# Optimization experiments

Measured on AMD Instinct MI355X. Metric: run time of the kernel, lower is better.

The kernel has to match this reference:

```python
import jax, jax.numpy as jnp
import numpy as np

SEQ, IN, H = 8192, 1024, 2048

def setup_inputs() -> dict:
    key = jax.random.key(0)
    ks = jax.random.split(key, 7)
    s = 0.02
    return {
        "input_seq": jax.random.normal(ks[0], (SEQ, IN), jnp.float32),
        "W_ih": jax.random.normal(ks[1], (4 * H, IN), jnp.float32) * s,
        "W_hh": jax.random.normal(ks[2], (4 * H, H), jnp.float32) * s,
        "b_ih": jax.random.normal(ks[3], (4 * H,), jnp.float32) * s,
        "b_hh": jax.random.normal(ks[4], (4 * H,), jnpp if False else jnp.float32) * s if False else jax.random.normal(ks[4], (4 * H,), jnp.float32) * s,
        "W_lin": jax.random.normal(ks[5], (1, H), jnp.float32) * s,
        "b_lin": jax.random.normal(ks[6], (1,), jnp.float32) * s,
    }

def _lstm(input_seq, W_ih, W_hh, b, H):
    # Precompute input projections for all timesteps: [S, 4H]
    x_proj = input_seq @ W_ih.T + b

    def step(carry, xp):
        h, c = carry
        gates = xp + h @ W_hh.T  # [4H], PyTorch order: i, f, g, o
        i = jax.nn.sigmoid(gates[0:H])
        f = jax.nn.sigmoid(gates[H:2 * H])
        g = jnp.tanh(gates[2 * H:3 * H])
        o = jax.nn.sigmoid(gates[3 * H:4 * H])
        c = f * c + i * g
        h = o * jnp.tanh(c)
        return (h, c), h

    h0 = jnp.zeros((H,), input_seq.dtype)
    c0 = jnp.zeros((H,), input_seq.dtype)
    _, hs = jax.lax.scan(step, (h0, c0), x_proj)
    return hs  # [S, H]

def reference(input_seq, W_ih, W_hh, b_ih, b_hh, W_lin, b_lin):
    H_ = W_hh.shape[1]
    hs = _lstm(input_seq, W_ih, W_hh, b_ih + b_hh, H_)
    # dropout is identity in eval mode; then linear + sigmoid + flatten
    out = jax.nn.sigmoid(hs @ W_lin.T + b_lin)  # [S, 1]
    return out.reshape(-1)
```

## Files before the change

### kernel.cpp

```cpp
#include <hip/hip_runtime.h>
#include <hip/hip_bf16.h>
#include <stdint.h>

constexpr int kSEQ = 8192;
constexpr int kIN  = 1024;
constexpr int kH   = 2048;
constexpr int kG4  = 4 * kH;
constexpr int kNB  = 256;
constexpr int kHB  = kH / kNB;
constexpr int kWP  = kH + 16;

constexpr size_t OFF_HBUF  = 0;
constexpr size_t OFF_ABORT = 32768;
constexpr size_t OFF_HS    = 65536;
constexpr size_t OFF_XP    = OFF_HS + (size_t)kSEQ * kH * 2;

__device__ __forceinline__ float bflo(uint32_t v) { return __uint_as_float(v << 16); }
__device__ __forceinline__ float bfhi(uint32_t v) { return __uint_as_float(v & 0xffff0000u); }

__global__ __launch_bounds__(256) void k_xproj(const float* __restrict__ A,
                                               const float* __restrict__ B,
                                               const float* __restrict__ bih,
                                               const float* __restrict__ bhh,
                                               __hip_bfloat16* __restrict__ C)
{
    __shared__ float As[16][65];
    __shared__ float Bs[16][65];

    const int bx = blockIdx.x & 127;
    const int by = blockIdx.x >> 7;
    const int tid = threadIdx.x;
    const int r  = tid >> 2;
    const int kq = (tid & 3) << 2;
    const int tx = tid & 15;
    const int ty = tid >> 4;
    const int m0 = by * 64, n0 = bx * 64;

    float acc[4][4] = {};

    for (int k0 = 0; k0 < kIN; k0 += 16) {
        float4 av = *(const float4*)&A[(size_t)(m0 + r) * kIN + k0 + kq];
        float4 bv = *(const float4*)&B[(size_t)(n0 + r) * kIN + k0 + kq];
        __syncthreads();
        As[kq + 0][r] = av.x; As[kq + 1][r] = av.y; As[kq + 2][r] = av.z; As[kq + 3][r] = av.w;
        Bs[kq + 0][r] = bv.x; Bs[kq + 1][r] = bv.y; Bs[kq + 2][r] = bv.z; Bs[kq + 3][r] = bv.w;
        __syncthreads();
        #pragma unroll
        for (int k = 0; k < 16; ++k) {
            float a0 = As[k][ty * 4 + 0], a1 = As[k][ty * 4 + 1];
            float a2 = As[k][ty * 4 + 2], a3 = As[k][ty * 4 + 3];
            float b0 = Bs[k][tx * 4 + 0], b1 = Bs[k][tx * 4 + 1];
            float b2 = Bs[k][tx * 4 + 2], b3 = Bs[k][tx * 4 + 3];
            acc[0][0] += a0 * b0; acc[0][1] += a0 * b1; acc[0][2] += a0 * b2; acc[0][3] += a0 * b3;
            acc[1][0] += a1 * b0; acc[1][1] += a1 * b1; acc[1][2] += a1 * b2; acc[1][3] += a1 * b3;
            acc[2][0] += a2 * b0; acc[2][1] += a2 * b1; acc[2][2] += a2 * b2; acc[2][3] += a2 * b3;
            acc[3][0] += a3 * b0; acc[3][1] += a3 * b1; acc[3][2] += a3 * b2; acc[3][3] += a3 * b3;
        }
    }

    #pragma unroll
    for (int i = 0; i < 4; ++i) {
        const int m = m0 + ty * 4 + i;
        #pragma unroll
        for (int j = 0; j < 4; ++j) {
            const int n = n0 + tx * 4 + j;
            C[(size_t)m * kG4 + n] = __float2bfloat16(acc[i][j] + bih[n] + bhh[n]);
        }
    }
}

__global__ __launch_bounds__(256, 1) void k_lstm(const float* __restrict__ Whh,
                                                 const __hip_bfloat16* __restrict__ xp,
                                                 unsigned long long* __restrict__ hbuf,
                                                 uint32_t* __restrict__ abortf,
                                                 __hip_bfloat16* __restrict__ hs)
{
    extern __shared__ char smem[];
    __hip_bfloat16* Wl  = (__hip_bfloat16*)smem;
    float*          hl2 = (float*)(smem + 32 * kWP * 2);

    const int wg  = blockIdx.x;
    const int tid = threadIdx.x;
    const int w   = tid >> 6;
    const int l   = tid & 63;
    const int hb  = wg * kHB;

    {
        const int lr = tid >> 3;
        const int g  = lr & 3;
        const int jl = 2 * (lr >> 3) + ((lr >> 2) & 1);
        const int cb = (tid & 7) * 256;
        const float* src = Whh + (size_t)(g * kH + hb + jl) * kH + cb;
        __hip_bfloat16* dst = Wl + (size_t)lr * kWP + cb;
        for (int c = 0; c < 256; c += 4) {
            float4 v = *(const float4*)(src + c);
            dst[c + 0] = __float2bfloat16(v.x);
            dst[c + 1] = __float2bfloat16(v.y);
            dst[c + 2] = __float2bfloat16(v.z);
            dst[c + 3] = __float2bfloat16(v.w);
        }
    }
    __syncthreads();

    const __hip_bfloat16* wrow = Wl + (size_t)(w * 8 + (l >> 3)) * kWP;
    const int kbase = (l & 7) * 8;
    const int jg = hb + 2 * w + (l >> 5);
    float c_state = 0.0f;
    uint32_t budget = 0;

    for (int t = 0; t < kSEQ; ++t) {
        const __hip_bfloat16* xr = xp + (size_t)t * kG4 + jg;
        const float xi = __bfloat162float(xr[0]);
        const float xf = __bfloat162float(xr[kH]);
        const float xg = __bfloat162float(xr[2 * kH]);
        const float xo = __bfloat162float(xr[3 * kH]);

        float* hw = hl2 + (size_t)(t & 1) * kH + tid * 8;
        int dead = 0;
        if (t == 0) {
            #pragma unroll
            for (int j = 0; j < 8; ++j) hw[j] = 0.f;
        } else {
            const unsigned long long* src = hbuf + (size_t)((t - 1) & 1) * kH + tid * 8;
            const uint32_t tag = (uint32_t)t;
            unsigned long long v[8];
            for (;;) {
                #pragma unroll
                for (int j = 0; j < 8; ++j)
                    v[j] = __hip_atomic_load(src + j, __ATOMIC_RELAXED, __HIP_MEMORY_SCOPE_AGENT);
                bool ok = true;
                #pragma unroll
                for (int j = 0; j < 8; ++j) ok &= ((uint32_t)v[j] == tag);
                if (ok) break;
                if ((++budget & 15) == 0) {
                    if (__hip_atomic_load(abortf, __ATOMIC_RELAXED,
                                          __HIP_MEMORY_SCOPE_AGENT) != 0u) { dead = 1; break; }
                    if (budget > (1u << 21)) {
                        __hip_atomic_store(abortf, 1u, __ATOMIC_RELAXED,
                                           __HIP_MEMORY_SCOPE_AGENT);
                        dead = 1; break;
                    }
                }
            }
            #pragma unroll
            for (int j = 0; j < 8; ++j) hw[j] = __uint_as_float((uint32_t)(v[j] >> 32));
        }
        if (__syncthreads_or(dead)) return;

        const float* hv = hl2 + (size_t)(t & 1) * kH;
        float acc = 0.f;
        #pragma unroll 8
        for (int it = 0; it < 32; ++it) {
            const int k = it * 64 + kbase;
            uint4 wv = *(const uint4*)(wrow + k);
            float4 h0 = *(const float4*)(hv + k);
            float4 h1 = *(const float4*)(hv + k + 4);
            acc += bflo(wv.x) * h0.x + bfhi(wv.x) * h0.y
                 + bflo(wv.y) * h0.z + bfhi(wv.y) * h0.w
                 + bflo(wv.z) * h1.x + bfhi(wv.z) * h1.y
                 + bflo(wv.w) * h1.z + bfhi(wv.w) * h1.w;
        }
        acc += __shfl_xor(acc, 1);
        acc += __shfl_xor(acc, 2);
        acc += __shfl_xor(acc, 4);

        const int base = l & 32;
        const float gi = __shfl(acc, base + 0)  + xi;
        const float gf = __shfl(acc, base + 8)  + xf;
        const float gg = __shfl(acc, base + 16) + xg;
        const float go = __shfl(acc, base + 24) + xo;
        const float si = 1.f / (1.f + expf(-gi));
        const float sf = 1.f / (1.f + expf(-gf));
        const float tg = tanhf(gg);
        const float so = 1.f / (1.f + expf(-go));
        c_state = sf * c_state + si * tg;
        const float hvv = so * tanhf(c_state);
        if ((l & 31) == 0) {
            hs[(size_t)t * kH + jg] = __float2bfloat16(hvv);
            const unsigned long long pv =
                ((unsigned long long)__float_as_uint(hvv) << 32) | (uint32_t)(t + 1);
            __hip_atomic_store(hbuf + (size_t)(t & 1) * kH + jg, pv,
                               __ATOMIC_RELAXED, __HIP_MEMORY_SCOPE_AGENT);
        }
    }
}

__global__ __launch_bounds__(256) void k_out(const __hip_bfloat16* __restrict__ hs,
                                             const float* __restrict__ wlin,
                                             const float* __restrict__ blin,
                                             float* __restrict__ out)
{
    const int w = threadIdx.x >> 6, l = threadIdx.x & 63;
    const int t = blockIdx.x * 4 + w;
    const __hip_bfloat16* row = hs + (size_t)t * kH;
    float acc = 0.f;
    #pragma unroll
    for (int i = 0; i < 4; ++i) {
        const int k = i * 512 + l * 8;
        uint4 hv = *(const uint4*)(row + k);
        float4 w0 = *(const float4*)(wlin + k);
        float4 w1 = *(const float4*)(wlin + k + 4);
        acc += bflo(hv.x) * w0.x + bfhi(hv.x) * w0.y
             + bflo(hv.y) * w0.z + bfhi(hv.y) * w0.w
             + bflo(hv.z) * w1.x + bfhi(hv.z) * w1.y
             + bflo(hv.w) * w1.z + bfhi(hv.w) * w1.w;
    }
    #pragma unroll
    for (int s = 32; s >= 1; s >>= 1) acc += __shfl_xor(acc, s);
    if (l == 0) out[t] = 1.f / (1.f + expf(-(acc + blin[0])));
}

extern "C" void kernel_launch(void* const* d_in, const int* in_sizes, int n_in,
                              void* d_out, int out_size, void* d_ws, size_t ws_size,
                              hipStream_t stream)
{
    const float* input_seq = (const float*)d_in[0];
    const float* W_ih      = (const float*)d_in[1];
    const float* W_hh      = (const float*)d_in[2];
    const float* b_ih      = (const float*)d_in[3];
    const float* b_hh      = (const float*)d_in[4];
    const float* W_lin     = (const float*)d_in[5];
    const float* b_lin     = (const float*)d_in[6];
    float* out = (float*)d_out;
    char*  ws  = (char*)d_ws;

    unsigned long long* hbuf = (unsigned long long*)(ws + OFF_HBUF);
    uint32_t*           abf  = (uint32_t*)(ws + OFF_ABORT);
    __hip_bfloat16*     hs   = (__hip_bfloat16*)(ws + OFF_HS);
    __hip_bfloat16*     xpb  = (__hip_bfloat16*)(ws + OFF_XP);

    hipMemsetAsync(ws, 0, 65536, stream);

    k_xproj<<<dim3(128 * 128), dim3(256), 0, stream>>>(input_seq, W_ih, b_ih, b_hh, xpb);

    constexpr int kLds = 32 * kWP * 2 + 2 * kH * 4;
    hipFuncSetAttribute((const void*)k_lstm, hipFuncAttributeMaxDynamicSharedMemorySize, kLds);

    {
        const float* a0 = W_hh; const __hip_bfloat16* a1 = xpb;
        unsigned long long* a2 = hbuf; uint32_t* a3 = abf; __hip_bfloat16* a4 = hs;
        void* args[5] = { &a0, &a1, &a2, &a3, &a4 };
        hipError_t ce = hipLaunchCooperativeKernel((const void*)k_lstm, dim3(kNB), dim3(256),
                                                   args, (unsigned)kLds, stream);
        if (ce != hipSuccess) {
            k_lstm<<<dim3(kNB), dim3(256), kLds, stream>>>(W_hh, xpb, hbuf, abf, hs);
        }
    }

    k_out<<<dim3(kSEQ / 4), dim3(256), 0, stream>>>(hs, W_lin, b_lin, out);
}
```

Before: 60.05 ms.

## Gate LSTM step on a global arrival counter before reading tagged h values

Adds a global atomic counter that every workgroup increments after publishing its h slice for a step. A single thread per workgroup polls that counter with s_sleep until all 256 groups have arrived, then all threads read the tagged hbuf once, with a per-element fallback spin. This replaces having every thread spin on 8 atomic loads, which is meant to cut polling traffic on the shared cache. It adds an extra __syncthreads and a contended atomic add per step, plus sleep latency on the critical path of a latency-bound recurrence.

```diff
diff --git a/kernel.cpp b/kernel.cpp
--- a/kernel.cpp
+++ b/kernel.cpp
@@ -12,6 +12,7 @@
 
 constexpr size_t OFF_HBUF  = 0;
 constexpr size_t OFF_ABORT = 32768;
+constexpr size_t OFF_CNT   = 33024;
 constexpr size_t OFF_HS    = 65536;
 constexpr size_t OFF_XP    = OFF_HS + (size_t)kSEQ * kH * 2;
 
@@ -73,6 +74,7 @@
                                                  const __hip_bfloat16* __restrict__ xp,
                                                  unsigned long long* __restrict__ hbuf,
                                                  uint32_t* __restrict__ abortf,
+                                                 uint32_t* __restrict__ cnt,
                                                  __hip_bfloat16* __restrict__ hs)
 {
     extern __shared__ char smem[];
@@ -120,32 +122,59 @@
         if (t == 0) {
             #pragma unroll
             for (int j = 0; j < 8; ++j) hw[j] = 0.f;
+            __syncthreads();
         } else {
+            if (tid == 0) {
+                const uint32_t want = (uint32_t)t * 256u;
+                for (;;) {
+                    uint32_t c = __hip_atomic_load(cnt, __ATOMIC_RELAXED,
+                                                   __HIP_MEMORY_SCOPE_AGENT);
+                    if (c >= want) break;
+                    __builtin_amdgcn_s_sleep(2);
+                    if ((++budget & 15) == 0) {
+                        if (__hip_atomic_load(abortf, __ATOMIC_RELAXED,
+                                              __HIP_MEMORY_SCOPE_AGENT) != 0u) { dead = 1; break; }
+                        if (budget > (1u << 20)) {
+                            __hip_atomic_store(abortf, 1u, __ATOMIC_RELAXED,
+                                               __HIP_MEMORY_SCOPE_AGENT);
+                            dead = 1; break;
+                        }
+                    }
+                }
+            }
+            if (__syncthreads_or(dead)) return;
+
             const unsigned long long* src = hbuf + (size_t)((t - 1) & 1) * kH + tid * 8;
             const uint32_t tag = (uint32_t)t;
             unsigned long long v[8];
-            for (;;) {
-                #pragma unroll
-                for (int j = 0; j < 8; ++j)
-                    v[j] = __hip_atomic_load(src + j, __ATOMIC_RELAXED, __HIP_MEMORY_SCOPE_AGENT);
-                bool ok = true;
-                #pragma unroll
-                for (int j = 0; j < 8; ++j) ok &= ((uint32_t)v[j] == tag);
-                if (ok) break;
-                if ((++budget & 15) == 0) {
-                    if (__hip_atomic_load(abortf, __ATOMIC_RELAXED,
-                                          __HIP_MEMORY_SCOPE_AGENT) != 0u) { dead = 1; break; }
-                    if (budget > (1u << 21)) {
-                        __hip_atomic_store(abortf, 1u, __ATOMIC_RELAXED,
-                                           __HIP_MEMORY_SCOPE_AGENT);
-                        dead = 1; break;
+            #pragma unroll
+            for (int j = 0; j < 8; ++j)
+                v[j] = __hip_atomic_load(src + j, __ATOMIC_RELAXED, __HIP_MEMORY_SCOPE_AGENT);
+            bool ok = true;
+            #pragma unroll
+            for (int j = 0; j < 8; ++j) ok &= ((uint32_t)v[j] == tag);
+            if (!ok) {
+                #pragma unroll 1
+                for (int j = 0; j < 8 && !dead; ++j) {
+                    while ((uint32_t)v[j] != tag) {
+                        v[j] = __hip_atomic_load(src + j, __ATOMIC_RELAXED,
+                                                 __HIP_MEMORY_SCOPE_AGENT);
+                        if ((++budget & 255) == 0) {
+                            if (__hip_atomic_load(abortf, __ATOMIC_RELAXED,
+                                                  __HIP_MEMORY_SCOPE_AGENT) != 0u ||
+                                budget > (1u << 20)) {
+                                __hip_atomic_store(abortf, 1u, __ATOMIC_RELAXED,
+                                                   __HIP_MEMORY_SCOPE_AGENT);
+                                dead = 1; break;
+                            }
+                        }
                     }
                 }
             }
             #pragma unroll
             for (int j = 0; j < 8; ++j) hw[j] = __uint_as_float((uint32_t)(v[j] >> 32));
-        }
-        if (__syncthreads_or(dead)) return;
+            if (__syncthreads_or(dead)) return;
+        }
 
         const float* hv = hl2 + (size_t)(t & 1) * kH;
         float acc = 0.f;
@@ -182,6 +211,9 @@
             __hip_atomic_store(hbuf + (size_t)(t & 1) * kH + jg, pv,
                                __ATOMIC_RELAXED, __HIP_MEMORY_SCOPE_AGENT);
         }
+        __syncthreads();
+        if (tid == 0)
+            __hip_atomic_fetch_add(cnt, 1u, __ATOMIC_RELAXED, __HIP_MEMORY_SCOPE_AGENT);
     }
 }
 
@@ -226,6 +258,7 @@
 
     unsigned long long* hbuf = (unsigned long long*)(ws + OFF_HBUF);
     uint32_t*           abf  = (uint32_t*)(ws + OFF_ABORT);
+    uint32_t*           cnt  = (uint32_t*)(ws + OFF_CNT);
     __hip_bfloat16*     hs   = (__hip_bfloat16*)(ws + OFF_HS);
     __hip_bfloat16*     xpb  = (__hip_bfloat16*)(ws + OFF_XP);
 
@@ -238,12 +271,13 @@
 
     {
         const float* a0 = W_hh; const __hip_bfloat16* a1 = xpb;
-        unsigned long long* a2 = hbuf; uint32_t* a3 = abf; __hip_bfloat16* a4 = hs;
-        void* args[5] = { &a0, &a1, &a2, &a3, &a4 };
+        unsigned long long* a2 = hbuf; uint32_t* a3 = abf; uint32_t* a4 = cnt;
+        __hip_bfloat16* a5 = hs;
+        void* args[6] = { &a0, &a1, &a2, &a3, &a4, &a5 };
         hipError_t ce = hipLaunchCooperativeKernel((const void*)k_lstm, dim3(kNB), dim3(256),
                                                    args, (unsigned)kLds, stream);
         if (ce != hipSuccess) {
-            k_lstm<<<dim3(kNB), dim3(256), kLds, stream>>>(W_hh, xpb, hbuf, abf, hs);
+            k_lstm<<<dim3(kNB), dim3(256), kLds, stream>>>(W_hh, xpb, hbuf, abf, cnt, hs);
         }
     }
 
```

After: 75.27 ms. 1.25x slower.

## Replace per-step block barrier with per-chunk LDS counters for streaming h consumption

Applied to the files above, without the earlier changes.

Removes the __syncthreads_or barrier after each wave loads its slice of the previous hidden state. In its place, every 8-thread group bumps a per-chunk LDS counter (double-buffered by step parity), and the dot-product loop spin-waits on each chunk's counter before reading it. The goal is to let waves start the matvec as soon as the chunks they need have arrived, so the global-poll latency overlaps with compute instead of serialising at a block barrier. The cost is extra LDS atomics and acquire loads inside the inner loop, a smaller unroll, and more complex abort handling.

```diff
diff --git a/kernel.cpp b/kernel.cpp
--- a/kernel.cpp
+++ b/kernel.cpp
@@ -76,14 +76,17 @@
                                                  __hip_bfloat16* __restrict__ hs)
 {
     extern __shared__ char smem[];
-    __hip_bfloat16* Wl  = (__hip_bfloat16*)smem;
-    float*          hl2 = (float*)(smem + 32 * kWP * 2);
+    __hip_bfloat16* Wl   = (__hip_bfloat16*)smem;
+    float*          hl2  = (float*)(smem + 32 * kWP * 2);
+    uint32_t*       cnts = (uint32_t*)(smem + 32 * kWP * 2 + 2 * kH * 4);
 
     const int wg  = blockIdx.x;
     const int tid = threadIdx.x;
     const int w   = tid >> 6;
     const int l   = tid & 63;
     const int hb  = wg * kHB;
+
+    if (tid < 64) cnts[tid] = 0;
 
     {
         const int lr = tid >> 3;
@@ -103,19 +106,23 @@
     __syncthreads();
 
     const __hip_bfloat16* wrow = Wl + (size_t)(w * 8 + (l >> 3)) * kWP;
-    const int kbase = (l & 7) * 8;
-    const int jg = hb + 2 * w + (l >> 5);
+    const int kbase   = (l & 7) * 8;
+    const int jg      = hb + 2 * w + (l >> 5);
+    const int mychunk = tid >> 3;
     float c_state = 0.0f;
     uint32_t budget = 0;
 
     for (int t = 0; t < kSEQ; ++t) {
+        const int b = t & 1;
+        const uint32_t tgt8 = 8u * ((uint32_t)(t >> 1) + 1u);
+
         const __hip_bfloat16* xr = xp + (size_t)t * kG4 + jg;
         const float xi = __bfloat162float(xr[0]);
         const float xf = __bfloat162float(xr[kH]);
         const float xg = __bfloat162float(xr[2 * kH]);
         const float xo = __bfloat162float(xr[3 * kH]);
 
-        float* hw = hl2 + (size_t)(t & 1) * kH + tid * 8;
+        float* hw = hl2 + (size_t)b * kH + tid * 8;
         int dead = 0;
         if (t == 0) {
             #pragma unroll
@@ -135,22 +142,40 @@
                 if ((++budget & 15) == 0) {
                     if (__hip_atomic_load(abortf, __ATOMIC_RELAXED,
                                           __HIP_MEMORY_SCOPE_AGENT) != 0u) { dead = 1; break; }
-                    if (budget > (1u << 21)) {
-                        __hip_atomic_store(abortf, 1u, __ATOMIC_RELAXED,
-                                           __HIP_MEMORY_SCOPE_AGENT);
-                        dead = 1; break;
-                    }
+                    if (budget > (1u << 21)) { dead = 1; break; }
                 }
             }
             #pragma unroll
             for (int j = 0; j < 8; ++j) hw[j] = __uint_as_float((uint32_t)(v[j] >> 32));
         }
-        if (__syncthreads_or(dead)) return;
-
-        const float* hv = hl2 + (size_t)(t & 1) * kH;
+        if (__any(dead)) {
+            __hip_atomic_store(abortf, 1u, __ATOMIC_RELAXED, __HIP_MEMORY_SCOPE_AGENT);
+            return;
+        }
+        __hip_atomic_fetch_add(&cnts[b * 32 + mychunk], 1u,
+                               __ATOMIC_RELEASE, __HIP_MEMORY_SCOPE_WORKGROUP);
+
+        const float* hv = hl2 + (size_t)b * kH;
         float acc = 0.f;
-        #pragma unroll 8
+        #pragma unroll 4
         for (int it = 0; it < 32; ++it) {
+            if (__hip_atomic_load(&cnts[b * 32 + it], __ATOMIC_ACQUIRE,
+                                  __HIP_MEMORY_SCOPE_WORKGROUP) < tgt8) {
+                int cdead = 0;
+                for (;;) {
+                    if (__hip_atomic_load(&cnts[b * 32 + it], __ATOMIC_ACQUIRE,
+                                          __HIP_MEMORY_SCOPE_WORKGROUP) >= tgt8) break;
+                    if ((++budget & 255) == 0) {
+                        if (__hip_atomic_load(abortf, __ATOMIC_RELAXED,
+                                              __HIP_MEMORY_SCOPE_AGENT) != 0u ||
+                            budget > (1u << 21)) { cdead = 1; break; }
+                    }
+                }
+                if (__any(cdead)) {
+                    __hip_atomic_store(abortf, 1u, __ATOMIC_RELAXED, __HIP_MEMORY_SCOPE_AGENT);
+                    return;
+                }
+            }
             const int k = it * 64 + kbase;
             uint4 wv = *(const uint4*)(wrow + k);
             float4 h0 = *(const float4*)(hv + k);
@@ -179,7 +204,7 @@
             hs[(size_t)t * kH + jg] = __float2bfloat16(hvv);
             const unsigned long long pv =
                 ((unsigned long long)__float_as_uint(hvv) << 32) | (uint32_t)(t + 1);
-            __hip_atomic_store(hbuf + (size_t)(t & 1) * kH + jg, pv,
+            __hip_atomic_store(hbuf + (size_t)b * kH + jg, pv,
                                __ATOMIC_RELAXED, __HIP_MEMORY_SCOPE_AGENT);
         }
     }
@@ -233,7 +258,7 @@
 
     k_xproj<<<dim3(128 * 128), dim3(256), 0, stream>>>(input_seq, W_ih, b_ih, b_hh, xpb);
 
-    constexpr int kLds = 32 * kWP * 2 + 2 * kH * 4;
+    constexpr int kLds = 32 * kWP * 2 + 2 * kH * 4 + 2 * 32 * 4;
     hipFuncSetAttribute((const void*)k_lstm, hipFuncAttributeMaxDynamicSharedMemorySize, kLds);
 
     {
```

Result: slower. 90.98 ms (+51.5%).
